# Kernel tuning notes

Hardware: AMD Instinct MI355X
Metric: run time of the kernel (lower is better)

## Reference

```python
import jax, jax.numpy as jnp
import numpy as np

N_NODES = 50000
N_EDGES = 800000
DIM = 128
HEADS = 8
DK = DIM // HEADS  # 16
SQRT_DK = float(np.sqrt(DK))


def setup_inputs() -> dict:
    key = jax.random.key(0)
    ks = jax.random.split(key, 12)
    inp = {
        "h": jax.random.normal(ks[0], (N_NODES, DIM), jnp.float32),
        "src": jax.random.randint(ks[1], (N_EDGES,), 0, N_NODES, jnp.int32),
        "dst": jax.random.randint(ks[2], (N_EDGES,), 0, N_NODES, jnp.int32),
        "Wk": jax.random.normal(ks[3], (DIM, DIM), jnp.float32) / np.sqrt(DIM),
        "bk": jnp.zeros((DIM,), jnp.float32),
        "Wq": jax.random.normal(ks[4], (DIM, DIM), jnp.float32) / np.sqrt(DIM),
        "bq": jnp.zeros((DIM,), jnp.float32),
        "Wv": jax.random.normal(ks[5], (DIM, DIM), jnp.float32) / np.sqrt(DIM),
        "bv": jnp.zeros((DIM,), jnp.float32),
        "Wa": jax.random.normal(ks[6], (DIM, DIM), jnp.float32) / np.sqrt(DIM),
        "ba": jnp.zeros((DIM,), jnp.float32),
        "rel_att": jax.random.normal(ks[7], (HEADS, DK, DK), jnp.float32) / np.sqrt(DK),
        "rel_msg": jax.random.normal(ks[8], (HEADS, DK, DK), jnp.float32) / np.sqrt(DK),
        "rel_pri": jnp.ones((HEADS,), jnp.float32),
        "skip": jnp.ones((1,), jnp.float32),
    }
    return inp


def reference(h, src, dst, Wk, bk, Wq, bq, Wv, bv, Wa, ba, rel_att, rel_msg, rel_pri, skip):
    N = h.shape[0]
    # node-level projections -> [N, H, d_k]
    k = (h @ Wk + bk).reshape(N, HEADS, DK)
    q = (h @ Wq + bq).reshape(N, HEADS, DK)
    v = (h @ Wv + bv).reshape(N, HEADS, DK)
    # relation-specific transforms
    k = jnp.einsum('nhi,hij->nhj', k, rel_att)
    v = jnp.einsum('nhi,hij->nhj', v, rel_msg)
    # per-edge score: dot(q[dst], k[src]) over d_k -> [E, H]
    score = jnp.einsum('ehd,ehd->eh', q[dst], k[src]) * rel_pri / SQRT_DK
    # segment softmax over destination nodes (edge_softmax, norm_by='dst')
    smax = jax.ops.segment_max(score, dst, num_segments=N)  # [N, H]
    e = jnp.exp(score - smax[dst])
    ssum = jax.ops.segment_sum(e, dst, num_segments=N)  # [N, H]
    attn = e / ssum[dst]  # [E, H]
    # weighted scatter-sum of messages: sum_e v[src_e] * attn_e -> [N, H, d_k]
    m = v[src] * attn[:, :, None]
    t = jax.ops.segment_sum(m, dst, num_segments=N).reshape(N, DIM)
    # target-specific aggregation (dropout in eval mode = identity, use_norm=False)
    trans_out = t @ Wa + ba
    alpha = jax.nn.sigmoid(skip)  # [1], broadcasts
    new_h = trans_out * alpha + h * (1.0 - alpha)
    return new_h
```

## Files before the change

### kernel.cpp

```cpp
#include <hip/hip_runtime.h>
#include <stdint.h>

#define NN 50000
#define NE 800000

typedef __bf16 v8bf __attribute__((ext_vector_type(8)));
typedef float  v4f  __attribute__((ext_vector_type(4)));
typedef unsigned short v8us __attribute__((ext_vector_type(8)));

#define EXP2F(x) __builtin_amdgcn_exp2f(x)

__device__ __forceinline__ float bf2f(unsigned short u) {
    return __uint_as_float(((unsigned)u) << 16);
}
__device__ __forceinline__ unsigned short f2bf(float f) {
    unsigned u = __float_as_uint(f);
    u += 0x7FFFu + ((u >> 16) & 1u);
    return (unsigned short)(u >> 16);
}
__device__ __forceinline__ float ldf(const void* p, size_t i, int isb) {
    return isb ? bf2f(((const unsigned short*)p)[i]) : ((const float*)p)[i];
}
__device__ __forceinline__ unsigned uminu(unsigned a, unsigned b) {
    return a < b ? a : b;
}

__global__ __launch_bounds__(128) void k_prep0(
    const void* __restrict__ Wq, const void* __restrict__ bq,
    const void* __restrict__ Wk, const void* __restrict__ bk,
    const void* __restrict__ Wv, const void* __restrict__ bv,
    const void* __restrict__ Wa, const void* __restrict__ ba,
    const void* __restrict__ rel_att, const void* __restrict__ rel_msg,
    const void* __restrict__ rel_pri,
    unsigned* __restrict__ CNTP,
    int* __restrict__ FLAG, unsigned short* __restrict__ WTb,
    float* __restrict__ BC)
{
    int b = blockIdx.x;
    int j = threadIdx.x;
    if (b >= 512) {
        unsigned idx = (unsigned)(b - 512) * 128u + (unsigned)j;
        uint4 z = make_uint4(0, 0, 0, 0);
        #pragma unroll
        for (int t = 0; t < 25; ++t) {
            unsigned o = idx + (unsigned)t * 8192u;
            if (o < 200004u) ((uint4*)CNTP)[o] = z;
        }
        return;
    }
    const unsigned rp0 = ((const unsigned*)rel_pri)[0];
    const int isb = ((rp0 & 0xFFFFu) != 0u) ? 1 : 0;
    int m = b >> 7;
    int i = b & 127;
    if (b == 0 && j == 0) FLAG[0] = isb;
    if (m == 0) {
        WTb[((size_t)(0 * 128 + j)) * 128 + i] = f2bf(ldf(Wq, i * 128 + j, isb));
        if (i == 0) BC[j] = ldf(bq, j, isb);
    } else if (m == 3) {
        WTb[((size_t)(3 * 128 + j)) * 128 + i] = f2bf(ldf(Wa, i * 128 + j, isb));
        if (i == 0) BC[3 * 128 + j] = ldf(ba, j, isb);
    } else {
        const void* W    = (m == 1) ? Wk : Wv;
        const void* bias = (m == 1) ? bk : bv;
        const void* R    = (m == 1) ? rel_att : rel_msg;
        int hh = j >> 4, jj = j & 15;
        float scale = (m == 1) ? ldf(rel_pri, hh, isb) * 0.25f : 1.0f;
        float acc = 0.f, bacc = 0.f;
        #pragma unroll
        for (int l = 0; l < 16; ++l) {
            float r = ldf(R, hh * 256 + l * 16 + jj, isb);
            acc  += ldf(W, i * 128 + hh * 16 + l, isb) * r;
            bacc += ldf(bias, hh * 16 + l, isb) * r;
        }
        WTb[((size_t)(m * 128 + j)) * 128 + i] = f2bf(acc * scale);
        if (i == 0) BC[m * 128 + j] = bacc * scale;
    }
}

#define NBG 391
#define NHB 3125
#define NSB 98
__global__ __launch_bounds__(256, 2) void k_qkvh(
    const void* __restrict__ h, const unsigned short* __restrict__ WTb,
    const float* __restrict__ BC, const int* __restrict__ FLAG,
    unsigned short* __restrict__ Qb, unsigned short* __restrict__ KVb,
    const int* __restrict__ dst,
    unsigned* __restrict__ CNTP, unsigned short* __restrict__ RANKS)
{
    __shared__ __align__(16) unsigned short Ah[128][136];
    __shared__ __align__(16) unsigned short Bh[128][136];
    const int tid = threadIdx.x;

    if (blockIdx.x >= NBG) {
        int e = (blockIdx.x - NBG) * 256 + tid;
        unsigned r = atomicAdd(&CNTP[(unsigned)dst[e] << 4], 1u);
        RANKS[e] = (unsigned short)r;
        return;
    }

    const int isb = FLAG[0];
    const int rowBase = blockIdx.x * 128;

    if (isb) {
        #pragma unroll
        for (int i = 0; i < 8; ++i) {
            int lin = tid + i * 256;
            int row = lin >> 4, kc = (lin & 15) * 8;
            int gr = rowBase + row;
            uint4 u = make_uint4(0, 0, 0, 0);
            if (gr < NN) u = *(const uint4*)((const unsigned short*)h + (size_t)gr * 128 + kc);
            *(uint4*)&Ah[row][kc] = u;
        }
    } else {
        #pragma unroll
        for (int i = 0; i < 16; ++i) {
            int lin = tid + i * 256;
            int row = lin >> 5, c4 = (lin & 31) * 4;
            int gr = rowBase + row;
            ushort4 o = make_ushort4(0, 0, 0, 0);
            if (gr < NN) {
                float4 f = *(const float4*)((const float*)h + (size_t)gr * 128 + c4);
                o.x = f2bf(f.x); o.y = f2bf(f.y); o.z = f2bf(f.z); o.w = f2bf(f.w);
            }
            *(ushort4*)&Ah[row][c4] = o;
        }
    }

    const int w = tid >> 6, l = tid & 63;
    const int lr = l & 15, q = l >> 4;
    v4f accK[2][8];

    for (int m = 0; m < 3; ++m) {
        if (m) __syncthreads();
        #pragma unroll
        for (int i = 0; i < 8; ++i) {
            int lin = tid + i * 256;
            int col = lin >> 4, kc = (lin & 15) * 8;
            uint4 u = *(const uint4*)(WTb + ((size_t)(m * 128 + col)) * 128 + kc);
            *(uint4*)&Bh[col][kc] = u;
        }
        __syncthreads();

        v4f acc[2][8];
        #pragma unroll
        for (int rt = 0; rt < 2; ++rt)
            #pragma unroll
            for (int nt = 0; nt < 8; ++nt) {
                float bj = BC[m * 128 + nt * 16 + lr];
                acc[rt][nt] = (v4f){bj, bj, bj, bj};
            }
        #pragma unroll
        for (int kk = 0; kk < 4; ++kk) {
            v8bf a0 = *(const v8bf*)&Ah[w * 32 +  0 + lr][kk * 32 + q * 8];
            v8bf a1 = *(const v8bf*)&Ah[w * 32 + 16 + lr][kk * 32 + q * 8];
            #pragma unroll
            for (int nt = 0; nt < 8; ++nt) {
                v8bf b = *(const v8bf*)&Bh[nt * 16 + lr][kk * 32 + q * 8];
                acc[0][nt] = __builtin_amdgcn_mfma_f32_16x16x32_bf16(a0, b, acc[0][nt], 0, 0, 0);
                acc[1][nt] = __builtin_amdgcn_mfma_f32_16x16x32_bf16(a1, b, acc[1][nt], 0, 0, 0);
            }
        }
        if (m == 0) {
            #pragma unroll
            for (int rt = 0; rt < 2; ++rt)
                #pragma unroll
                for (int nt = 0; nt < 8; ++nt)
                    #pragma unroll
                    for (int r = 0; r < 4; ++r) {
                        int row = rowBase + w * 32 + rt * 16 + q * 4 + r;
                        if (row < NN)
                            Qb[(size_t)row * 128 + nt * 16 + lr] = f2bf(acc[rt][nt][r]);
                    }
        } else if (m == 1) {
            #pragma unroll
            for (int rt = 0; rt < 2; ++rt)
                #pragma unroll
                for (int nt = 0; nt < 8; ++nt) accK[rt][nt] = acc[rt][nt];
        } else {
            #pragma unroll
            for (int rt = 0; rt < 2; ++rt)
                #pragma unroll
                for (int nt = 0; nt < 8; ++nt)
                    #pragma unroll
                    for (int r = 0; r < 4; ++r) {
                        int row = rowBase + w * 32 + rt * 16 + q * 4 + r;
                        if (row < NN) {
                            ushort2 kv;
                            kv.x = f2bf(accK[rt][nt][r]);
                            kv.y = f2bf(acc[rt][nt][r]);
                            *(ushort2*)&KVb[(size_t)row * 256 + (nt * 16 + lr) * 2] = kv;
                        }
                    }
        }
    }
}

__global__ __launch_bounds__(256) void k_scan(
    const unsigned* __restrict__ CNTP,
    unsigned* __restrict__ RPS, unsigned* __restrict__ BSUM,
    unsigned* __restrict__ BOFF, unsigned* __restrict__ DONE)
{
    __shared__ unsigned shs[256];
    __shared__ int lastFlag;
    const int tid = threadIdx.x;
    int sb = blockIdx.x;
    int g0 = sb * 512 + tid * 2, g1 = g0 + 1;
    unsigned v0 = (g0 < NN) ? CNTP[(size_t)g0 << 4] : 0u;
    unsigned v1 = (g1 < NN) ? CNTP[(size_t)g1 << 4] : 0u;
    unsigned pv = v0 + v1;
    shs[tid] = pv;
    __syncthreads();
    #pragma unroll
    for (int off = 1; off < 256; off <<= 1) {
        unsigned t = 0;
        if (tid >= off) t = shs[tid - off];
        __syncthreads();
        if (tid >= off) shs[tid] += t;
        __syncthreads();
    }
    unsigned excl = shs[tid] - pv;
    if (g0 < NN) RPS[g0] = excl;
    if (g1 < NN) RPS[g1] = excl + v0;
    if (tid == 255) atomicExch(&BSUM[sb], shs[255]);
    __syncthreads();
    if (tid == 0) {
        __threadfence();
        lastFlag = (atomicAdd(DONE, 1u) == NSB - 1);
    }
    __syncthreads();
    if (!lastFlag) return;
    unsigned bv = (tid < NSB) ? atomicAdd(&BSUM[tid], 0u) : 0u;
    __syncthreads();
    shs[tid] = bv;
    __syncthreads();
    #pragma unroll
    for (int off = 1; off < 256; off <<= 1) {
        unsigned t = 0;
        if (tid >= off) t = shs[tid - off];
        __syncthreads();
        if (tid >= off) shs[tid] += t;
        __syncthreads();
    }
    if (tid < NSB) BOFF[tid] = shs[tid] - bv;
}

__global__ __launch_bounds__(256) void k_fill(
    const int* __restrict__ src, const int* __restrict__ dst,
    const unsigned short* __restrict__ RANKS,
    const unsigned* __restrict__ RPS, const unsigned* __restrict__ BOFF,
    unsigned short* __restrict__ ESRC, unsigned* __restrict__ ROW)
{
    int t = blockIdx.x * 256 + threadIdx.x;
    if (t < NN) ROW[t] = RPS[t] + BOFF[t >> 9];
    if (t >= NE / 2) return;
    int e = t * 2;
    const int2 d2 = *(const int2*)(dst + e);
    const int2 s2 = *(const int2*)(src + e);
    const ushort2 r2 = *(const ushort2*)(RANKS + e);
    unsigned p0 = RPS[d2.x] + BOFF[d2.x >> 9] + r2.x;
    unsigned p1 = RPS[d2.y] + BOFF[d2.y >> 9] + r2.y;
    ESRC[p0] = (unsigned short)s2.x;
    ESRC[p1] = (unsigned short)s2.y;
}

__global__ __launch_bounds__(256) void k_attn(
    const unsigned* __restrict__ ROW,
    const unsigned short* __restrict__ ESRC,
    const unsigned short* __restrict__ Qb, const unsigned short* __restrict__ KVb,
    unsigned short* __restrict__ Tb)
{
    int d = (blockIdx.x * 256 + threadIdx.x) >> 6;
    int lane = threadIdx.x & 63;
    int hl = lane >> 5;
    int sub = lane & 31;
    const float LOG2E = 1.4426950408889634f;

    unsigned beg = ROW[d];
    unsigned end = (d == NN - 1) ? (unsigned)NE : ROW[d + 1];

    const ushort4 qu = *(const ushort4*)(Qb + (size_t)d * 128 + sub * 4);
    float q0 = bf2f(qu.x) * LOG2E, q1 = bf2f(qu.y) * LOG2E;
    float q2 = bf2f(qu.z) * LOG2E, q3 = bf2f(qu.w) * LOG2E;

    float s = 0.f, o0 = 0.f, o1 = 0.f, o2 = 0.f, o3 = 0.f;
    int n = (int)(end - beg);

#define ATT_F(kv) {                                                         \
        float p = q0 * bf2f(kv[0]) + q1 * bf2f(kv[2])                       \
                + q2 * bf2f(kv[4]) + q3 * bf2f(kv[6]);                      \
        p += __shfl_xor(p, 1);                                              \
        p += __shfl_xor(p, 2);                                              \
        float wgt = EXP2F(p);                                               \
        s  += wgt;                                                          \
        o0 += wgt * bf2f(kv[1]); o1 += wgt * bf2f(kv[3]);                   \
        o2 += wgt * bf2f(kv[5]); o3 += wgt * bf2f(kv[7]); }
#define ATT_T(kv, idx) {                                                    \
        float p = q0 * bf2f(kv[0]) + q1 * bf2f(kv[2])                       \
                + q2 * bf2f(kv[4]) + q3 * bf2f(kv[6]);                      \
        p += __shfl_xor(p, 1);                                              \
        p += __shfl_xor(p, 2);                                              \
        float wgt = ((idx) < end) ? EXP2F(p) : 0.f;                         \
        s  += wgt;                                                          \
        o0 += wgt * bf2f(kv[1]); o1 += wgt * bf2f(kv[3]);                   \
        o2 += wgt * bf2f(kv[5]); o3 += wgt * bf2f(kv[7]); }
#define GATH(sid) (*(const v8us*)(KVB + (((unsigned)(sid) << 9) + voff)))

    if (n > 0) {
        const unsigned char* KVB = (const unsigned char*)KVb;
        const unsigned voff = (unsigned)(sub * 16);
        const unsigned last = end - 1;
        const int RT = (n + 7) >> 3;
        const int tail = n & 7;
        const unsigned b0 = beg + (unsigned)hl;

        unsigned sA0 = ESRC[uminu(b0 + 0u, last)];
        unsigned sA1 = ESRC[uminu(b0 + 2u, last)];
        unsigned sA2 = ESRC[uminu(b0 + 4u, last)];
        unsigned sA3 = ESRC[uminu(b0 + 6u, last)];
        v8us kA0 = GATH(sA0), kA1 = GATH(sA1), kA2 = GATH(sA2), kA3 = GATH(sA3);
        unsigned sB0 = 0, sB1 = 0, sB2 = 0, sB3 = 0;
        if (RT > 1) {
            unsigned b1 = b0 + 8u;
            sB0 = ESRC[uminu(b1 + 0u, last)];
            sB1 = ESRC[uminu(b1 + 2u, last)];
            sB2 = ESRC[uminu(b1 + 4u, last)];
            sB3 = ESRC[uminu(b1 + 6u, last)];
        }

        for (int r = 0; r < RT; ++r) {
            v8us kB0 = kA0, kB1 = kA1, kB2 = kA2, kB3 = kA3;
            if (r + 1 < RT) {
                kB0 = GATH(sB0); kB1 = GATH(sB1);
                kB2 = GATH(sB2); kB3 = GATH(sB3);
            }
            unsigned sC0 = sB0, sC1 = sB1, sC2 = sB2, sC3 = sB3;
            if (r + 2 < RT) {
                unsigned b2 = b0 + (unsigned)(8 * (r + 2));
                sC0 = ESRC[uminu(b2 + 0u, last)];
                sC1 = ESRC[uminu(b2 + 2u, last)];
                sC2 = ESRC[uminu(b2 + 4u, last)];
                sC3 = ESRC[uminu(b2 + 6u, last)];
            }
            if (r == RT - 1 && tail) {
                unsigned base = beg + (unsigned)(8 * r) + (unsigned)hl;
                ATT_T(kA0, base + 0u);
                ATT_T(kA1, base + 2u);
                ATT_T(kA2, base + 4u);
                ATT_T(kA3, base + 6u);
            } else {
                ATT_F(kA0); ATT_F(kA1); ATT_F(kA2); ATT_F(kA3);
            }
            kA0 = kB0; kA1 = kB1; kA2 = kB2; kA3 = kB3;
            sB0 = sC0; sB1 = sC1; sB2 = sC2; sB3 = sC3;
        }
    }
#undef ATT_F
#undef ATT_T
#undef GATH

    s  += __shfl_xor(s, 32);
    o0 += __shfl_xor(o0, 32);
    o1 += __shfl_xor(o1, 32);
    o2 += __shfl_xor(o2, 32);
    o3 += __shfl_xor(o3, 32);
    float r = (s > 0.f) ? (1.0f / s) : 0.f;
    if (hl == 0) {
        ushort4 o;
        o.x = f2bf(o0 * r); o.y = f2bf(o1 * r);
        o.z = f2bf(o2 * r); o.w = f2bf(o3 * r);
        *(ushort4*)(Tb + (size_t)d * 128 + sub * 4) = o;
    }
}

__global__ __launch_bounds__(256, 2) void k_final_m(
    const unsigned short* __restrict__ Tb, const unsigned short* __restrict__ WTb,
    const float* __restrict__ BC, const void* __restrict__ h,
    const void* __restrict__ skip, const int* __restrict__ FLAG,
    void* __restrict__ out)
{
    __shared__ __align__(16) unsigned short Ah[128][136];
    __shared__ __align__(16) unsigned short Bh[128][136];
    const int isb = FLAG[0];
    const int tid = threadIdx.x;
    const int rowBase = blockIdx.x * 128;

    #pragma unroll
    for (int i = 0; i < 8; ++i) {
        int lin = tid + i * 256;
        int row = lin >> 4, kc = (lin & 15) * 8;
        int gr = rowBase + row;
        uint4 u = make_uint4(0, 0, 0, 0);
        if (gr < NN) u = *(const uint4*)(Tb + (size_t)gr * 128 + kc);
        *(uint4*)&Ah[row][kc] = u;
    }
    #pragma unroll
    for (int i = 0; i < 8; ++i) {
        int lin = tid + i * 256;
        int col = lin >> 4, kc = (lin & 15) * 8;
        uint4 u = *(const uint4*)(WTb + ((size_t)(3 * 128 + col)) * 128 + kc);
        *(uint4*)&Bh[col][kc] = u;
    }
    __syncthreads();

    const int w = tid >> 6, l = tid & 63;
    const int lr = l & 15, q = l >> 4;
    v4f acc[2][8];
    #pragma unroll
    for (int rt = 0; rt < 2; ++rt)
        #pragma unroll
        for (int nt = 0; nt < 8; ++nt) {
            float bj = BC[3 * 128 + nt * 16 + lr];
            acc[rt][nt] = (v4f){bj, bj, bj, bj};
        }
    #pragma unroll
    for (int kk = 0; kk < 4; ++kk) {
        v8bf a0 = *(const v8bf*)&Ah[w * 32 +  0 + lr][kk * 32 + q * 8];
        v8bf a1 = *(const v8bf*)&Ah[w * 32 + 16 + lr][kk * 32 + q * 8];
        #pragma unroll
        for (int nt = 0; nt < 8; ++nt) {
            v8bf b = *(const v8bf*)&Bh[nt * 16 + lr][kk * 32 + q * 8];
            acc[0][nt] = __builtin_amdgcn_mfma_f32_16x16x32_bf16(a0, b, acc[0][nt], 0, 0, 0);
            acc[1][nt] = __builtin_amdgcn_mfma_f32_16x16x32_bf16(a1, b, acc[1][nt], 0, 0, 0);
        }
    }
    float skipv = ldf(skip, 0, isb);
    float alpha = 1.0f / (1.0f + __expf(-skipv));
    float beta = 1.0f - alpha;
    #pragma unroll
    for (int rt = 0; rt < 2; ++rt)
        #pragma unroll
        for (int nt = 0; nt < 8; ++nt) {
            #pragma unroll
            for (int r = 0; r < 4; ++r) {
                int row = rowBase + w * 32 + rt * 16 + q * 4 + r;
                if (row < NN) {
                    size_t off = (size_t)row * 128 + nt * 16 + lr;
                    float hv = ldf(h, off, isb);
                    float o = alpha * acc[rt][nt][r] + beta * hv;
                    if (isb) ((unsigned short*)out)[off] = f2bf(o);
                    else     ((float*)out)[off] = o;
                }
            }
        }
}

extern "C" void kernel_launch(void* const* d_in, const int* in_sizes, int n_in,
                              void* d_out, int out_size, void* d_ws, size_t ws_size,
                              hipStream_t stream)
{
    const void* h  = d_in[0];
    const int* src = (const int*)d_in[1];
    const int* dst = (const int*)d_in[2];
    const void* Wk = d_in[3];
    const void* bk = d_in[4];
    const void* Wq = d_in[5];
    const void* bq = d_in[6];
    const void* Wv = d_in[7];
    const void* bv = d_in[8];
    const void* Wa = d_in[9];
    const void* ba = d_in[10];
    const void* rel_att = d_in[11];
    const void* rel_msg = d_in[12];
    const void* rel_pri = d_in[13];
    const void* skip    = d_in[14];

    float* F = (float*)d_ws;
    int* FLAG      = (int*)F;
    float* BC      = F + 16;
    unsigned short* WTb = (unsigned short*)(BC + 512);
    unsigned* CNTP = (unsigned*)((float*)(BC + 512) + 32768);
    unsigned* DONE = CNTP + 800000;
    unsigned short* RANKS = (unsigned short*)(DONE + 16);
    unsigned* RPS  = (unsigned*)(RANKS + 800000);
    unsigned* BSUM = RPS + 50048;
    unsigned* BOFF = BSUM + 128;
    unsigned* ROW  = BOFF + 128;
    unsigned short* Tb = (unsigned short*)(ROW + 50048);
    unsigned short* ESRC = Tb + (size_t)NN * 128;
    unsigned short* Qb  = ESRC + NE;
    unsigned short* KVb = Qb + (size_t)NN * 128;

    k_prep0<<<512 + 64, 128, 0, stream>>>(Wq, bq, Wk, bk, Wv, bv, Wa, ba,
                                          rel_att, rel_msg, rel_pri,
                                          CNTP, FLAG, WTb, BC);
    k_qkvh<<<NBG + NHB, 256, 0, stream>>>(h, WTb, BC, FLAG, Qb, KVb,
                                          dst, CNTP, RANKS);
    k_scan<<<NSB, 256, 0, stream>>>(CNTP, RPS, BSUM, BOFF, DONE);
    k_fill<<<(NE / 2 + 255) / 256, 256, 0, stream>>>(src, dst, RANKS, RPS, BOFF, ESRC, ROW);
    k_attn<<<(NN * 64) / 256, 256, 0, stream>>>(ROW, ESRC, Qb, KVb, Tb);
    k_final_m<<<NBG, 256, 0, stream>>>(Tb, WTb, BC, h, skip, FLAG, d_out);
}
```

Measured before the change: 241.0 us.

## Drop LDS staging in projection GEMMs; load MFMA operands directly from global

Both the QKV projection and the final output projection now skip the shared-memory tiles. Each wave loads its A fragments straight from global into registers and reads the weight fragments directly from global (cache-resident) for every MFMA. The row tile shrinks from 128 to 64 per block, the grid doubles to match, and the occupancy hint in launch bounds is removed. This is meant to remove LDS staging, the barriers and the LDS limit on occupancy. The cost is redundant global/L2 reads of the weight matrix in every wave and smaller tiles with less reuse.

```diff
diff --git a/kernel.cpp b/kernel.cpp
--- a/kernel.cpp
+++ b/kernel.cpp
@@ -24,6 +24,7 @@
 __device__ __forceinline__ unsigned uminu(unsigned a, unsigned b) {
     return a < b ? a : b;
 }
+union bcast8 { v8us u; v8bf b; };
 
 __global__ __launch_bounds__(128) void k_prep0(
     const void* __restrict__ Wq, const void* __restrict__ bq,
@@ -77,18 +78,16 @@
     }
 }
 
-#define NBG 391
+#define NBG 782
 #define NHB 3125
 #define NSB 98
-__global__ __launch_bounds__(256, 2) void k_qkvh(
+__global__ __launch_bounds__(256) void k_qkvh(
     const void* __restrict__ h, const unsigned short* __restrict__ WTb,
     const float* __restrict__ BC, const int* __restrict__ FLAG,
     unsigned short* __restrict__ Qb, unsigned short* __restrict__ KVb,
     const int* __restrict__ dst,
     unsigned* __restrict__ CNTP, unsigned short* __restrict__ RANKS)
 {
-    __shared__ __align__(16) unsigned short Ah[128][136];
-    __shared__ __align__(16) unsigned short Bh[128][136];
     const int tid = threadIdx.x;
 
     if (blockIdx.x >= NBG) {
@@ -99,98 +98,78 @@
     }
 
     const int isb = FLAG[0];
-    const int rowBase = blockIdx.x * 128;
-
-    if (isb) {
-        #pragma unroll
-        for (int i = 0; i < 8; ++i) {
-            int lin = tid + i * 256;
-            int row = lin >> 4, kc = (lin & 15) * 8;
-            int gr = rowBase + row;
-            uint4 u = make_uint4(0, 0, 0, 0);
-            if (gr < NN) u = *(const uint4*)((const unsigned short*)h + (size_t)gr * 128 + kc);
-            *(uint4*)&Ah[row][kc] = u;
-        }
-    } else {
-        #pragma unroll
-        for (int i = 0; i < 16; ++i) {
-            int lin = tid + i * 256;
-            int row = lin >> 5, c4 = (lin & 31) * 4;
-            int gr = rowBase + row;
-            ushort4 o = make_ushort4(0, 0, 0, 0);
-            if (gr < NN) {
-                float4 f = *(const float4*)((const float*)h + (size_t)gr * 128 + c4);
-                o.x = f2bf(f.x); o.y = f2bf(f.y); o.z = f2bf(f.z); o.w = f2bf(f.w);
-            }
-            *(ushort4*)&Ah[row][c4] = o;
-        }
-    }
-
+    const int rowBase = blockIdx.x * 64;
     const int w = tid >> 6, l = tid & 63;
     const int lr = l & 15, q = l >> 4;
-    v4f accK[2][8];
-
+
+    int arow = rowBase + w * 16 + lr;
+    int crow = (arow < NN) ? arow : (NN - 1);
+    v8bf a[4];
+    if (isb) {
+        const unsigned short* hp = (const unsigned short*)h + (size_t)crow * 128 + q * 8;
+        #pragma unroll
+        for (int kk = 0; kk < 4; ++kk) {
+            bcast8 c; c.u = *(const v8us*)(hp + kk * 32);
+            a[kk] = c.b;
+        }
+    } else {
+        const float* hp = (const float*)h + (size_t)crow * 128 + q * 8;
+        #pragma unroll
+        for (int kk = 0; kk < 4; ++kk) {
+            float4 f0 = *(const float4*)(hp + kk * 32);
+            float4 f1 = *(const float4*)(hp + kk * 32 + 4);
+            bcast8 c;
+            c.u[0] = f2bf(f0.x); c.u[1] = f2bf(f0.y);
+            c.u[2] = f2bf(f0.z); c.u[3] = f2bf(f0.w);
+            c.u[4] = f2bf(f1.x); c.u[5] = f2bf(f1.y);
+            c.u[6] = f2bf(f1.z); c.u[7] = f2bf(f1.w);
+            a[kk] = c.b;
+        }
+    }
+
+    v4f accK[8];
     for (int m = 0; m < 3; ++m) {
-        if (m) __syncthreads();
-        #pragma unroll
-        for (int i = 0; i < 8; ++i) {
-            int lin = tid + i * 256;
-            int col = lin >> 4, kc = (lin & 15) * 8;
-            uint4 u = *(const uint4*)(WTb + ((size_t)(m * 128 + col)) * 128 + kc);
-            *(uint4*)&Bh[col][kc] = u;
-        }
-        __syncthreads();
-
-        v4f acc[2][8];
-        #pragma unroll
-        for (int rt = 0; rt < 2; ++rt)
+        v4f acc[8];
+        #pragma unroll
+        for (int nt = 0; nt < 8; ++nt) {
+            float bj = BC[m * 128 + nt * 16 + lr];
+            acc[nt] = (v4f){bj, bj, bj, bj};
+        }
+        #pragma unroll
+        for (int kk = 0; kk < 4; ++kk) {
             #pragma unroll
             for (int nt = 0; nt < 8; ++nt) {
-                float bj = BC[m * 128 + nt * 16 + lr];
-                acc[rt][nt] = (v4f){bj, bj, bj, bj};
-            }
-        #pragma unroll
-        for (int kk = 0; kk < 4; ++kk) {
-            v8bf a0 = *(const v8bf*)&Ah[w * 32 +  0 + lr][kk * 32 + q * 8];
-            v8bf a1 = *(const v8bf*)&Ah[w * 32 + 16 + lr][kk * 32 + q * 8];
-            #pragma unroll
-            for (int nt = 0; nt < 8; ++nt) {
-                v8bf b = *(const v8bf*)&Bh[nt * 16 + lr][kk * 32 + q * 8];
-                acc[0][nt] = __builtin_amdgcn_mfma_f32_16x16x32_bf16(a0, b, acc[0][nt], 0, 0, 0);
-                acc[1][nt] = __builtin_amdgcn_mfma_f32_16x16x32_bf16(a1, b, acc[1][nt], 0, 0, 0);
+                bcast8 bb;
+                bb.u = *(const v8us*)(WTb + ((size_t)(m * 128 + nt * 16 + lr)) * 128
+                                      + kk * 32 + q * 8);
+                acc[nt] = __builtin_amdgcn_mfma_f32_16x16x32_bf16(a[kk], bb.b, acc[nt], 0, 0, 0);
             }
         }
         if (m == 0) {
             #pragma unroll
-            for (int rt = 0; rt < 2; ++rt)
+            for (int nt = 0; nt < 8; ++nt)
                 #pragma unroll
-                for (int nt = 0; nt < 8; ++nt)
-                    #pragma unroll
-                    for (int r = 0; r < 4; ++r) {
-                        int row = rowBase + w * 32 + rt * 16 + q * 4 + r;
-                        if (row < NN)
-                            Qb[(size_t)row * 128 + nt * 16 + lr] = f2bf(acc[rt][nt][r]);
-                    }
+                for (int r = 0; r < 4; ++r) {
+                    int row = rowBase + w * 16 + q * 4 + r;
+                    if (row < NN)
+                        Qb[(size_t)row * 128 + nt * 16 + lr] = f2bf(acc[nt][r]);
+                }
         } else if (m == 1) {
             #pragma unroll
-            for (int rt = 0; rt < 2; ++rt)
-                #pragma unroll
-                for (int nt = 0; nt < 8; ++nt) accK[rt][nt] = acc[rt][nt];
+            for (int nt = 0; nt < 8; ++nt) accK[nt] = acc[nt];
         } else {
             #pragma unroll
-            for (int rt = 0; rt < 2; ++rt)
+            for (int nt = 0; nt < 8; ++nt)
                 #pragma unroll
-                for (int nt = 0; nt < 8; ++nt)
-                    #pragma unroll
-                    for (int r = 0; r < 4; ++r) {
-                        int row = rowBase + w * 32 + rt * 16 + q * 4 + r;
-                        if (row < NN) {
-                            ushort2 kv;
-                            kv.x = f2bf(accK[rt][nt][r]);
-                            kv.y = f2bf(acc[rt][nt][r]);
-                            *(ushort2*)&KVb[(size_t)row * 256 + (nt * 16 + lr) * 2] = kv;
-                        }
+                for (int r = 0; r < 4; ++r) {
+                    int row = rowBase + w * 16 + q * 4 + r;
+                    if (row < NN) {
+                        ushort2 kv;
+                        kv.x = f2bf(accK[nt][r]);
+                        kv.y = f2bf(acc[nt][r]);
+                        *(ushort2*)&KVb[(size_t)row * 256 + (nt * 16 + lr) * 2] = kv;
                     }
+                }
         }
     }
 }
@@ -372,76 +351,63 @@
     }
 }
 
-__global__ __launch_bounds__(256, 2) void k_final_m(
+__global__ __launch_bounds__(256) void k_final_m(
     const unsigned short* __restrict__ Tb, const unsigned short* __restrict__ WTb,
     const float* __restrict__ BC, const void* __restrict__ h,
     const void* __restrict__ skip, const int* __restrict__ FLAG,
     void* __restrict__ out)
 {
-    __shared__ __align__(16) unsigned short Ah[128][136];
-    __shared__ __align__(16) unsigned short Bh[128][136];
     const int isb = FLAG[0];
     const int tid = threadIdx.x;
-    const int rowBase = blockIdx.x * 128;
-
-    #pragma unroll
-    for (int i = 0; i < 8; ++i) {
-        int lin = tid + i * 256;
-        int row = lin >> 4, kc = (lin & 15) * 8;
-        int gr = rowBase + row;
-        uint4 u = make_uint4(0, 0, 0, 0);
-        if (gr < NN) u = *(const uint4*)(Tb + (size_t)gr * 128 + kc);
-        *(uint4*)&Ah[row][kc] = u;
-    }
-    #pragma unroll
-    for (int i = 0; i < 8; ++i) {
-        int lin = tid + i * 256;
-        int col = lin >> 4, kc = (lin & 15) * 8;
-        uint4 u = *(const uint4*)(WTb + ((size_t)(3 * 128 + col)) * 128 + kc);
-        *(uint4*)&Bh[col][kc] = u;
-    }
-    __syncthreads();
-
+    const int rowBase = blockIdx.x * 64;
     const int w = tid >> 6, l = tid & 63;
     const int lr = l & 15, q = l >> 4;
-    v4f acc[2][8];
+
+    int arow = rowBase + w * 16 + lr;
+    int crow = (arow < NN) ? arow : (NN - 1);
+    v8bf a[4];
+    {
+        const unsigned short* tp = Tb + (size_t)crow * 128 + q * 8;
+        #pragma unroll
+        for (int kk = 0; kk < 4; ++kk) {
+            bcast8 c; c.u = *(const v8us*)(tp + kk * 32);
+            a[kk] = c.b;
+        }
+    }
+
+    v4f acc[8];
     #pragma unroll
-    for (int rt = 0; rt < 2; ++rt)
-        #pragma unroll
-        for (int nt = 0; nt < 8; ++nt) {
-            float bj = BC[3 * 128 + nt * 16 + lr];
-            acc[rt][nt] = (v4f){bj, bj, bj, bj};
-        }
+    for (int nt = 0; nt < 8; ++nt) {
+        float bj = BC[3 * 128 + nt * 16 + lr];
+        acc[nt] = (v4f){bj, bj, bj, bj};
+    }
     #pragma unroll
     for (int kk = 0; kk < 4; ++kk) {
-        v8bf a0 = *(const v8bf*)&Ah[w * 32 +  0 + lr][kk * 32 + q * 8];
-        v8bf a1 = *(const v8bf*)&Ah[w * 32 + 16 + lr][kk * 32 + q * 8];
         #pragma unroll
         for (int nt = 0; nt < 8; ++nt) {
-            v8bf b = *(const v8bf*)&Bh[nt * 16 + lr][kk * 32 + q * 8];
-            acc[0][nt] = __builtin_amdgcn_mfma_f32_16x16x32_bf16(a0, b, acc[0][nt], 0, 0, 0);
-            acc[1][nt] = __builtin_amdgcn_mfma_f32_16x16x32_bf16(a1, b, acc[1][nt], 0, 0, 0);
+            bcast8 bb;
+            bb.u = *(const v8us*)(WTb + ((size_t)(3 * 128 + nt * 16 + lr)) * 128
+                                  + kk * 32 + q * 8);
+            acc[nt] = __builtin_amdgcn_mfma_f32_16x16x32_bf16(a[kk], bb.b, acc[nt], 0, 0, 0);
         }
     }
     float skipv = ldf(skip, 0, isb);
     float alpha = 1.0f / (1.0f + __expf(-skipv));
     float beta = 1.0f - alpha;
     #pragma unroll
-    for (int rt = 0; rt < 2; ++rt)
-        #pragma unroll
-        for (int nt = 0; nt < 8; ++nt) {
-            #pragma unroll
-            for (int r = 0; r < 4; ++r) {
-                int row = rowBase + w * 32 + rt * 16 + q * 4 + r;
-                if (row < NN) {
-                    size_t off = (size_t)row * 128 + nt * 16 + lr;
-                    float hv = ldf(h, off, isb);
-                    float o = alpha * acc[rt][nt][r] + beta * hv;
-                    if (isb) ((unsigned short*)out)[off] = f2bf(o);
-                    else     ((float*)out)[off] = o;
-                }
+    for (int nt = 0; nt < 8; ++nt) {
+        #pragma unroll
+        for (int r = 0; r < 4; ++r) {
+            int row = rowBase + w * 16 + q * 4 + r;
+            if (row < NN) {
+                size_t off = (size_t)row * 128 + nt * 16 + lr;
+                float hv = ldf(h, off, isb);
+                float o = alpha * acc[nt][r] + beta * hv;
+                if (isb) ((unsigned short*)out)[off] = f2bf(o);
+                else     ((float*)out)[off] = o;
             }
         }
+    }
 }
 
 extern "C" void kernel_launch(void* const* d_in, const int* in_sizes, int n_in,
```

Result: slower. 262.1 us (+8.8%).

## Merge six kernel launches into two cooperative persistent kernels with grid syncs

Applied to the files above, without the earlier changes.

Replaces the chain of six separate kernel launches with two cooperative persistent kernels. Each one iterates over the former blocks' work items and uses grid.sync between stages, so inter-kernel launch gaps and tail drain are removed. If a cooperative launch fails, the code falls back to the separate kernels. The final GEMM also moves to 64-row tiles that read the Wa operand straight from global memory instead of staging it in LDS. In exchange, the fixed grid of 512 or 1024 blocks may reduce occupancy or load balance in the attention and GEMM stages, and each grid sync adds its own cost.

```diff
diff --git a/kernel.cpp b/kernel.cpp
--- a/kernel.cpp
+++ b/kernel.cpp
@@ -1,8 +1,15 @@
 #include <hip/hip_runtime.h>
+#include <hip/hip_cooperative_groups.h>
 #include <stdint.h>
+
+namespace cg = cooperative_groups;
 
 #define NN 50000
 #define NE 800000
+#define NBG 391
+#define NHB 3125
+#define NSB 98
+#define NFB 782
 
 typedef __bf16 v8bf __attribute__((ext_vector_type(8)));
 typedef float  v4f  __attribute__((ext_vector_type(4)));
@@ -24,20 +31,16 @@
 __device__ __forceinline__ unsigned uminu(unsigned a, unsigned b) {
     return a < b ? a : b;
 }
-
-__global__ __launch_bounds__(128) void k_prep0(
-    const void* __restrict__ Wq, const void* __restrict__ bq,
-    const void* __restrict__ Wk, const void* __restrict__ bk,
-    const void* __restrict__ Wv, const void* __restrict__ bv,
-    const void* __restrict__ Wa, const void* __restrict__ ba,
-    const void* __restrict__ rel_att, const void* __restrict__ rel_msg,
-    const void* __restrict__ rel_pri,
-    unsigned* __restrict__ CNTP,
-    int* __restrict__ FLAG, unsigned short* __restrict__ WTb,
-    float* __restrict__ BC)
-{
-    int b = blockIdx.x;
-    int j = threadIdx.x;
+union bcast8 { v8us u; v8bf b; };
+
+
+__device__ __forceinline__ void dev_prep(
+    int b, int j,
+    const void* Wq, const void* bq, const void* Wk, const void* bk,
+    const void* Wv, const void* bv, const void* Wa, const void* ba,
+    const void* rel_att, const void* rel_msg, const void* rel_pri,
+    unsigned* CNTP, int* FLAG, unsigned short* WTb, float* BC)
+{
     if (b >= 512) {
         unsigned idx = (unsigned)(b - 512) * 128u + (unsigned)j;
         uint4 z = make_uint4(0, 0, 0, 0);
@@ -77,30 +80,20 @@
     }
 }
 
-#define NBG 391
-#define NHB 3125
-#define NSB 98
-__global__ __launch_bounds__(256, 2) void k_qkvh(
-    const void* __restrict__ h, const unsigned short* __restrict__ WTb,
-    const float* __restrict__ BC, const int* __restrict__ FLAG,
-    unsigned short* __restrict__ Qb, unsigned short* __restrict__ KVb,
-    const int* __restrict__ dst,
-    unsigned* __restrict__ CNTP, unsigned short* __restrict__ RANKS)
-{
-    __shared__ __align__(16) unsigned short Ah[128][136];
-    __shared__ __align__(16) unsigned short Bh[128][136];
-    const int tid = threadIdx.x;
-
-    if (blockIdx.x >= NBG) {
-        int e = (blockIdx.x - NBG) * 256 + tid;
-        unsigned r = atomicAdd(&CNTP[(unsigned)dst[e] << 4], 1u);
-        RANKS[e] = (unsigned short)r;
-        return;
-    }
-
+__device__ __forceinline__ void dev_hist(
+    int e, const int* dst, unsigned* CNTP, unsigned short* RANKS)
+{
+    unsigned r = atomicAdd(&CNTP[(unsigned)dst[e] << 4], 1u);
+    RANKS[e] = (unsigned short)r;
+}
+
+__device__ __forceinline__ void dev_gemm_qkv(
+    int rowBase, int tid,
+    unsigned short (*Ah)[136], unsigned short (*Bh)[136],
+    const void* h, const unsigned short* WTb, const float* BC,
+    const int* FLAG, unsigned short* Qb, unsigned short* KVb)
+{
     const int isb = FLAG[0];
-    const int rowBase = blockIdx.x * 128;
-
     if (isb) {
         #pragma unroll
         for (int i = 0; i < 8; ++i) {
@@ -195,15 +188,11 @@
     }
 }
 
-__global__ __launch_bounds__(256) void k_scan(
-    const unsigned* __restrict__ CNTP,
-    unsigned* __restrict__ RPS, unsigned* __restrict__ BSUM,
-    unsigned* __restrict__ BOFF, unsigned* __restrict__ DONE)
-{
-    __shared__ unsigned shs[256];
-    __shared__ int lastFlag;
-    const int tid = threadIdx.x;
-    int sb = blockIdx.x;
+__device__ __forceinline__ void dev_scan(
+    int sb, int tid, unsigned* shs, int* lastFlagP,
+    const unsigned* CNTP, unsigned* RPS, unsigned* BSUM,
+    unsigned* BOFF, unsigned* DONE)
+{
     int g0 = sb * 512 + tid * 2, g1 = g0 + 1;
     unsigned v0 = (g0 < NN) ? CNTP[(size_t)g0 << 4] : 0u;
     unsigned v1 = (g1 < NN) ? CNTP[(size_t)g1 << 4] : 0u;
@@ -225,52 +214,51 @@
     __syncthreads();
     if (tid == 0) {
         __threadfence();
-        lastFlag = (atomicAdd(DONE, 1u) == NSB - 1);
+        *lastFlagP = (atomicAdd(DONE, 1u) == NSB - 1);
     }
     __syncthreads();
-    if (!lastFlag) return;
-    unsigned bv = (tid < NSB) ? atomicAdd(&BSUM[tid], 0u) : 0u;
+    if (*lastFlagP) {
+        unsigned bv = (tid < NSB) ? atomicAdd(&BSUM[tid], 0u) : 0u;
+        __syncthreads();
+        shs[tid] = bv;
+        __syncthreads();
+        #pragma unroll
+        for (int off = 1; off < 256; off <<= 1) {
+            unsigned t = 0;
+            if (tid >= off) t = shs[tid - off];
+            __syncthreads();
+            if (tid >= off) shs[tid] += t;
+            __syncthreads();
+        }
+        if (tid < NSB) BOFF[tid] = shs[tid] - bv;
+    }
     __syncthreads();
-    shs[tid] = bv;
-    __syncthreads();
-    #pragma unroll
-    for (int off = 1; off < 256; off <<= 1) {
-        unsigned t = 0;
-        if (tid >= off) t = shs[tid - off];
-        __syncthreads();
-        if (tid >= off) shs[tid] += t;
-        __syncthreads();
-    }
-    if (tid < NSB) BOFF[tid] = shs[tid] - bv;
-}
-
-__global__ __launch_bounds__(256) void k_fill(
-    const int* __restrict__ src, const int* __restrict__ dst,
-    const unsigned short* __restrict__ RANKS,
-    const unsigned* __restrict__ RPS, const unsigned* __restrict__ BOFF,
-    unsigned short* __restrict__ ESRC, unsigned* __restrict__ ROW)
-{
-    int t = blockIdx.x * 256 + threadIdx.x;
+}
+
+__device__ __forceinline__ void dev_fill(
+    int t, const int* src, const int* dst, const unsigned short* RANKS,
+    const unsigned* RPS, const unsigned* BOFF,
+    unsigned short* ESRC, unsigned* ROW)
+{
     if (t < NN) ROW[t] = RPS[t] + BOFF[t >> 9];
-    if (t >= NE / 2) return;
-    int e = t * 2;
-    const int2 d2 = *(const int2*)(dst + e);
-    const int2 s2 = *(const int2*)(src + e);
-    const ushort2 r2 = *(const ushort2*)(RANKS + e);
-    unsigned p0 = RPS[d2.x] + BOFF[d2.x >> 9] + r2.x;
-    unsigned p1 = RPS[d2.y] + BOFF[d2.y >> 9] + r2.y;
-    ESRC[p0] = (unsigned short)s2.x;
-    ESRC[p1] = (unsigned short)s2.y;
-}
-
-__global__ __launch_bounds__(256) void k_attn(
-    const unsigned* __restrict__ ROW,
-    const unsigned short* __restrict__ ESRC,
-    const unsigned short* __restrict__ Qb, const unsigned short* __restrict__ KVb,
-    unsigned short* __restrict__ Tb)
-{
-    int d = (blockIdx.x * 256 + threadIdx.x) >> 6;
-    int lane = threadIdx.x & 63;
+    if (t < NE / 2) {
+        int e = t * 2;
+        const int2 d2 = *(const int2*)(dst + e);
+        const int2 s2 = *(const int2*)(src + e);
+        const ushort2 r2 = *(const ushort2*)(RANKS + e);
+        unsigned p0 = RPS[d2.x] + BOFF[d2.x >> 9] + r2.x;
+        unsigned p1 = RPS[d2.y] + BOFF[d2.y >> 9] + r2.y;
+        ESRC[p0] = (unsigned short)s2.x;
+        ESRC[p1] = (unsigned short)s2.y;
+    }
+}
+
+__device__ __forceinline__ void dev_attn(
+    int d, int lane,
+    const unsigned* ROW, const unsigned short* ESRC,
+    const unsigned short* Qb, const unsigned short* KVb,
+    unsigned short* Tb)
+{
     int hl = lane >> 5;
     int sub = lane & 31;
     const float LOG2E = 1.4426950408889634f;
@@ -372,20 +360,14 @@
     }
 }
 
-__global__ __launch_bounds__(256, 2) void k_final_m(
-    const unsigned short* __restrict__ Tb, const unsigned short* __restrict__ WTb,
-    const float* __restrict__ BC, const void* __restrict__ h,
-    const void* __restrict__ skip, const int* __restrict__ FLAG,
-    void* __restrict__ out)
-{
-    __shared__ __align__(16) unsigned short Ah[128][136];
-    __shared__ __align__(16) unsigned short Bh[128][136];
+__device__ __forceinline__ void dev_final(
+    int rowBase, int tid, unsigned short (*Ah)[136],
+    const unsigned short* Tb, const unsigned short* WTb, const float* BC,
+    const void* h, const void* skip, const int* FLAG, void* out)
+{
     const int isb = FLAG[0];
-    const int tid = threadIdx.x;
-    const int rowBase = blockIdx.x * 128;
-
     #pragma unroll
-    for (int i = 0; i < 8; ++i) {
+    for (int i = 0; i < 4; ++i) {
         int lin = tid + i * 256;
         int row = lin >> 4, kc = (lin & 15) * 8;
         int gr = rowBase + row;
@@ -393,55 +375,169 @@
         if (gr < NN) u = *(const uint4*)(Tb + (size_t)gr * 128 + kc);
         *(uint4*)&Ah[row][kc] = u;
     }
-    #pragma unroll
-    for (int i = 0; i < 8; ++i) {
-        int lin = tid + i * 256;
-        int col = lin >> 4, kc = (lin & 15) * 8;
-        uint4 u = *(const uint4*)(WTb + ((size_t)(3 * 128 + col)) * 128 + kc);
-        *(uint4*)&Bh[col][kc] = u;
-    }
     __syncthreads();
 
     const int w = tid >> 6, l = tid & 63;
     const int lr = l & 15, q = l >> 4;
-    v4f acc[2][8];
+
+    v8bf a[4];
     #pragma unroll
-    for (int rt = 0; rt < 2; ++rt)
-        #pragma unroll
-        for (int nt = 0; nt < 8; ++nt) {
-            float bj = BC[3 * 128 + nt * 16 + lr];
-            acc[rt][nt] = (v4f){bj, bj, bj, bj};
-        }
+    for (int kk = 0; kk < 4; ++kk)
+        a[kk] = *(const v8bf*)&Ah[w * 16 + lr][kk * 32 + q * 8];
+
+    v4f acc[8];
+    #pragma unroll
+    for (int nt = 0; nt < 8; ++nt) {
+        float bj = BC[3 * 128 + nt * 16 + lr];
+        acc[nt] = (v4f){bj, bj, bj, bj};
+    }
     #pragma unroll
     for (int kk = 0; kk < 4; ++kk) {
-        v8bf a0 = *(const v8bf*)&Ah[w * 32 +  0 + lr][kk * 32 + q * 8];
-        v8bf a1 = *(const v8bf*)&Ah[w * 32 + 16 + lr][kk * 32 + q * 8];
         #pragma unroll
         for (int nt = 0; nt < 8; ++nt) {
-            v8bf b = *(const v8bf*)&Bh[nt * 16 + lr][kk * 32 + q * 8];
-            acc[0][nt] = __builtin_amdgcn_mfma_f32_16x16x32_bf16(a0, b, acc[0][nt], 0, 0, 0);
-            acc[1][nt] = __builtin_amdgcn_mfma_f32_16x16x32_bf16(a1, b, acc[1][nt], 0, 0, 0);
+            bcast8 bb;
+            bb.u = *(const v8us*)(WTb + ((size_t)(3 * 128 + nt * 16 + lr)) * 128
+                                  + kk * 32 + q * 8);
+            acc[nt] = __builtin_amdgcn_mfma_f32_16x16x32_bf16(a[kk], bb.b, acc[nt], 0, 0, 0);
         }
     }
     float skipv = ldf(skip, 0, isb);
     float alpha = 1.0f / (1.0f + __expf(-skipv));
     float beta = 1.0f - alpha;
     #pragma unroll
-    for (int rt = 0; rt < 2; ++rt)
-        #pragma unroll
-        for (int nt = 0; nt < 8; ++nt) {
-            #pragma unroll
-            for (int r = 0; r < 4; ++r) {
-                int row = rowBase + w * 32 + rt * 16 + q * 4 + r;
-                if (row < NN) {
-                    size_t off = (size_t)row * 128 + nt * 16 + lr;
-                    float hv = ldf(h, off, isb);
-                    float o = alpha * acc[rt][nt][r] + beta * hv;
-                    if (isb) ((unsigned short*)out)[off] = f2bf(o);
-                    else     ((float*)out)[off] = o;
-                }
+    for (int nt = 0; nt < 8; ++nt) {
+        #pragma unroll
+        for (int r = 0; r < 4; ++r) {
+            int row = rowBase + w * 16 + q * 4 + r;
+            if (row < NN) {
+                size_t off = (size_t)row * 128 + nt * 16 + lr;
+                float hv = ldf(h, off, isb);
+                float o = alpha * acc[nt][r] + beta * hv;
+                if (isb) ((unsigned short*)out)[off] = f2bf(o);
+                else     ((float*)out)[off] = o;
             }
         }
+    }
+}
+
+__global__ __launch_bounds__(256, 2) void k_pipe1(
+    const void* Wq, const void* bq, const void* Wk, const void* bk,
+    const void* Wv, const void* bv, const void* Wa, const void* ba,
+    const void* rel_att, const void* rel_msg, const void* rel_pri,
+    const void* h, const int* dst, int* FLAG, unsigned short* WTb, float* BC,
+    unsigned* CNTP, unsigned short* RANKS, unsigned short* Qb, unsigned short* KVb,
+    unsigned* RPS, unsigned* BSUM, unsigned* BOFF, unsigned* DONE)
+{
+    cg::grid_group grid = cg::this_grid();
+    __shared__ __align__(16) unsigned short Ah[128][136];
+    __shared__ __align__(16) unsigned short Bh[128][136];
+    __shared__ int lastFlag;
+    const int tid = threadIdx.x;
+    const int nb = gridDim.x;
+
+    for (int wi = blockIdx.x; wi < 288; wi += nb) {
+        int b = wi * 2 + (tid >> 7);
+        dev_prep(b, tid & 127, Wq, bq, Wk, bk, Wv, bv, Wa, ba,
+                 rel_att, rel_msg, rel_pri, CNTP, FLAG, WTb, BC);
+    }
+    grid.sync();
+
+    for (int wi = blockIdx.x; wi < NBG + NHB; wi += nb) {
+        if (wi < NBG) {
+            dev_gemm_qkv(wi * 128, tid, Ah, Bh, h, WTb, BC, FLAG, Qb, KVb);
+            __syncthreads();
+        } else {
+            dev_hist((wi - NBG) * 256 + tid, dst, CNTP, RANKS);
+        }
+    }
+    grid.sync();
+
+    unsigned* shs = (unsigned*)&Ah[0][0];
+    for (int wi = blockIdx.x; wi < NSB; wi += nb)
+        dev_scan(wi, tid, shs, &lastFlag, CNTP, RPS, BSUM, BOFF, DONE);
+}
+
+__global__ __launch_bounds__(256, 4) void k_pipe2(
+    const int* src, const int* dst, const unsigned short* RANKS,
+    const unsigned* RPS, const unsigned* BOFF,
+    unsigned short* ESRC, unsigned* ROW,
+    const unsigned short* Qb, const unsigned short* KVb, unsigned short* Tb,
+    const unsigned short* WTb, const float* BC, const void* h,
+    const void* skip, const int* FLAG, void* out)
+{
+    cg::grid_group grid = cg::this_grid();
+    __shared__ __align__(16) unsigned short Ah[64][136];
+    const int tid = threadIdx.x;
+    const int nb = gridDim.x;
+
+    for (int wi = blockIdx.x; wi < 1563; wi += nb)
+        dev_fill(wi * 256 + tid, src, dst, RANKS, RPS, BOFF, ESRC, ROW);
+    grid.sync();
+
+    for (int wi = blockIdx.x; wi < 12500; wi += nb)
+        dev_attn(wi * 4 + (tid >> 6), tid & 63, ROW, ESRC, Qb, KVb, Tb);
+    grid.sync();
+
+    for (int wi = blockIdx.x; wi < NFB; wi += nb) {
+        dev_final(wi * 64, tid, Ah, Tb, WTb, BC, h, skip, FLAG, out);
+        __syncthreads();
+    }
+}
+
+__global__ __launch_bounds__(128) void k_prep0c(
+    const void* Wq, const void* bq, const void* Wk, const void* bk,
+    const void* Wv, const void* bv, const void* Wa, const void* ba,
+    const void* rel_att, const void* rel_msg, const void* rel_pri,
+    unsigned* CNTP, int* FLAG, unsigned short* WTb, float* BC)
+{
+    dev_prep(blockIdx.x, threadIdx.x, Wq, bq, Wk, bk, Wv, bv, Wa, ba,
+             rel_att, rel_msg, rel_pri, CNTP, FLAG, WTb, BC);
+}
+
+__global__ __launch_bounds__(256, 2) void k_qkvhc(
+    const void* h, const unsigned short* WTb, const float* BC, const int* FLAG,
+    unsigned short* Qb, unsigned short* KVb,
+    const int* dst, unsigned* CNTP, unsigned short* RANKS)
+{
+    __shared__ __align__(16) unsigned short Ah[128][136];
+    __shared__ __align__(16) unsigned short Bh[128][136];
+    if (blockIdx.x < NBG)
+        dev_gemm_qkv(blockIdx.x * 128, threadIdx.x, Ah, Bh, h, WTb, BC, FLAG, Qb, KVb);
+    else
+        dev_hist((blockIdx.x - NBG) * 256 + threadIdx.x, dst, CNTP, RANKS);
+}
+
+__global__ __launch_bounds__(256) void k_scanc(
+    const unsigned* CNTP, unsigned* RPS, unsigned* BSUM,
+    unsigned* BOFF, unsigned* DONE)
+{
+    __shared__ unsigned shs[256];
+    __shared__ int lastFlag;
+    dev_scan(blockIdx.x, threadIdx.x, shs, &lastFlag, CNTP, RPS, BSUM, BOFF, DONE);
+}
+
+__global__ __launch_bounds__(256) void k_fillc(
+    const int* src, const int* dst, const unsigned short* RANKS,
+    const unsigned* RPS, const unsigned* BOFF,
+    unsigned short* ESRC, unsigned* ROW)
+{
+    dev_fill(blockIdx.x * 256 + threadIdx.x, src, dst, RANKS, RPS, BOFF, ESRC, ROW);
+}
+
+__global__ __launch_bounds__(256) void k_attnc(
+    const unsigned* ROW, const unsigned short* ESRC,
+    const unsigned short* Qb, const unsigned short* KVb, unsigned short* Tb)
+{
+    dev_attn((blockIdx.x * 256 + threadIdx.x) >> 6, threadIdx.x & 63,
+             ROW, ESRC, Qb, KVb, Tb);
+}
+
+__global__ __launch_bounds__(256) void k_finalc(
+    const unsigned short* Tb, const unsigned short* WTb, const float* BC,
+    const void* h, const void* skip, const int* FLAG, void* out)
+{
+    __shared__ __align__(16) unsigned short Ah[64][136];
+    dev_final(blockIdx.x * 64, threadIdx.x, Ah, Tb, WTb, BC, h, skip, FLAG, out);
 }
 
 extern "C" void kernel_launch(void* const* d_in, const int* in_sizes, int n_in,
@@ -480,13 +576,34 @@
     unsigned short* Qb  = ESRC + NE;
     unsigned short* KVb = Qb + (size_t)NN * 128;
 
-    k_prep0<<<512 + 64, 128, 0, stream>>>(Wq, bq, Wk, bk, Wv, bv, Wa, ba,
+    void* p1[] = {
+        (void*)&Wq, (void*)&bq, (void*)&Wk, (void*)&bk,
+        (void*)&Wv, (void*)&bv, (void*)&Wa, (void*)&ba,
+        (void*)&rel_att, (void*)&rel_msg, (void*)&rel_pri,
+        (void*)&h, (void*)&dst, (void*)&FLAG, (void*)&WTb, (void*)&BC,
+        (void*)&CNTP, (void*)&RANKS, (void*)&Qb, (void*)&KVb,
+        (void*)&RPS, (void*)&BSUM, (void*)&BOFF, (void*)&DONE };
+    hipError_t e1 = hipLaunchCooperativeKernel((void*)k_pipe1, dim3(512),
+                                               dim3(256), p1, 0, stream);
+    if (e1 != hipSuccess) {
+        k_prep0c<<<576, 128, 0, stream>>>(Wq, bq, Wk, bk, Wv, bv, Wa, ba,
                                           rel_att, rel_msg, rel_pri,
                                           CNTP, FLAG, WTb, BC);
-    k_qkvh<<<NBG + NHB, 256, 0, stream>>>(h, WTb, BC, FLAG, Qb, KVb,
-                                          dst, CNTP, RANKS);
-    k_scan<<<NSB, 256, 0, stream>>>(CNTP, RPS, BSUM, BOFF, DONE);
-    k_fill<<<(NE / 2 + 255) / 256, 256, 0, stream>>>(src, dst, RANKS, RPS, BOFF, ESRC, ROW);
-    k_attn<<<(NN * 64) / 256, 256, 0, stream>>>(ROW, ESRC, Qb, KVb, Tb);
-    k_final_m<<<NBG, 256, 0, stream>>>(Tb, WTb, BC, h, skip, FLAG, d_out);
-}
+        k_qkvhc<<<NBG + NHB, 256, 0, stream>>>(h, WTb, BC, FLAG, Qb, KVb,
+                                               dst, CNTP, RANKS);
+        k_scanc<<<NSB, 256, 0, stream>>>(CNTP, RPS, BSUM, BOFF, DONE);
+    }
+
+    void* p2[] = {
+        (void*)&src, (void*)&dst, (void*)&RANKS, (void*)&RPS, (void*)&BOFF,
+        (void*)&ESRC, (void*)&ROW, (void*)&Qb, (void*)&KVb, (void*)&Tb,
+        (void*)&WTb, (void*)&BC, (void*)&h, (void*)&skip, (void*)&FLAG,
+        (void*)&d_out };
+    hipError_t e2 = hipLaunchCooperativeKernel((void*)k_pipe2, dim3(1024),
+                                               dim3(256), p2, 0, stream);
+    if (e2 != hipSuccess) {
+        k_fillc<<<1563, 256, 0, stream>>>(src, dst, RANKS, RPS, BOFF, ESRC, ROW);
+        k_attnc<<<12500, 256, 0, stream>>>(ROW, ESRC, Qb, KVb, Tb);
+        k_finalc<<<NFB, 256, 0, stream>>>(Tb, WTb, BC, h, skip, FLAG, d_out);
+    }
+}
```

Result: slower. 670.7 us (+178.3%).
